# Kernel tuning notes

Hardware: AMD Instinct MI355X
Metric: run time of the kernel (lower is better)

The kernel has to match this reference:

```python
import jax, jax.numpy as jnp
import numpy as np

BEV_H = 150; BEV_W = 150; D = 4; NCAM = 6; C = 128
FH = 48; FW = 88            # camera feature map size
IMG_H = 480.0; IMG_W = 800.0  # raw image size used to normalize uv
PC = np.array([-51.2, -51.2, -5.0, 51.2, 51.2, 3.0], np.float32)  # pc_range


def setup_inputs() -> dict:
    key = jax.random.key(0)
    # GenerateGrid buffer: (D, 3, h, w) with channels (x, y, z), normalized to [0,1]
    z = PC[5] - PC[2]
    zs = (np.linspace(0.5, z - 0.5, D) / z).astype(np.float32)
    xs = (np.linspace(0.5, BEV_W - 0.5, BEV_W) / BEV_W).astype(np.float32)
    ys = (np.linspace(0.5, BEV_H - 0.5, BEV_H) / BEV_H).astype(np.float32)
    g = np.zeros((D, 3, BEV_H, BEV_W), np.float32)
    g[:, 0] = xs[None, None, :]
    g[:, 1] = ys[None, :, None]
    g[:, 2] = zs[:, None, None]
    # realistic surround-camera rig: 6 cams looking outward every 60 deg
    I = np.zeros((1, NCAM, 3, 3), np.float32)
    E = np.zeros((1, NCAM, 4, 4), np.float32)
    for i in range(NCAM):
        I[0, i] = [[500.0, 0.0, 400.0], [0.0, 500.0, 240.0], [0.0, 0.0, 1.0]]
        yaw = 2.0 * np.pi * i / NCAM
        fwd = np.array([np.cos(yaw), np.sin(yaw), 0.0])
        right = np.array([np.sin(yaw), -np.cos(yaw), 0.0])
        down = np.array([0.0, 0.0, -1.0])
        R = np.stack([right, down, fwd])  # rows = camera axes in ego frame
        campos = np.array([1.5 * np.cos(yaw), 1.5 * np.sin(yaw), 1.5])
        E[0, i, :3, :3] = R
        E[0, i, :3, 3] = -R @ campos
        E[0, i, 3, 3] = 1.0
    feat = jax.random.normal(key, (1, NCAM, FH, FW, C), jnp.float32)
    return {"feat": feat, "I": jnp.asarray(I), "E": jnp.asarray(E), "grid_3d": jnp.asarray(g)}


def _forward(feat, I, E, grid_3d):
    b, n = I.shape[:2]
    d, _, h, w = grid_3d.shape
    Q = h * w
    scale = jnp.asarray([PC[3] - PC[0], PC[4] - PC[1], PC[5] - PC[2]], feat.dtype)
    off = jnp.asarray([PC[0], PC[1], PC[2]], feat.dtype)
    # (D, Q, 3) ego-frame 3D reference points, then homogeneous (D, Q, 4)
    rp = grid_3d.reshape(d, 3, Q).transpose(0, 2, 1) * scale + off
    rp4 = jnp.concatenate([rp, jnp.ones((d, Q, 1), rp.dtype)], axis=-1)
    # lidar2img = I @ E[:, :, :3, :] -> (b, n, 3, 4); project -> (b, n, D, Q, 3)
    l2i = jnp.einsum('bnij,bnjk->bnik', I, E[:, :, :3, :])
    proj = jnp.einsum('bnij,dqj->bndqi', l2i, rp4)
    eps = 1e-5
    zc = proj[..., 2]
    mask = zc > eps
    uv = proj[..., :2] / jnp.maximum(zc, eps)[..., None]
    u = uv[..., 0] / IMG_W
    v = uv[..., 1] / IMG_H
    mask = mask & (u > 0.0) & (u < 1.0) & (v > 0.0) & (v < 1.0)
    # bilinear grid_sample (align_corners=False, zero padding) at (u, v)
    px = u * FW - 0.5
    py = v * FH - 0.5
    x0 = jnp.floor(px)
    y0 = jnp.floor(py)
    wx1 = px - x0; wy1 = py - y0
    wx0 = 1.0 - wx1; wy0 = 1.0 - wy1
    x0i = x0.astype(jnp.int32)
    y0i = y0.astype(jnp.int32)
    ff = feat.reshape(b, n, FH * FW, C)

    def gather(xi, yi, wt):
        valid = (xi >= 0) & (xi < FW) & (yi >= 0) & (yi < FH)
        idx = (jnp.clip(yi, 0, FH - 1) * FW + jnp.clip(xi, 0, FW - 1)).reshape(b, n, d * Q)
        g = jnp.take_along_axis(ff, idx[..., None], axis=2).reshape(b, n, d, Q, C)
        return g * (wt * valid.astype(feat.dtype))[..., None]

    sampled = (gather(x0i, y0i, wx0 * wy0) + gather(x0i + 1, y0i, wx1 * wy0)
               + gather(x0i, y0i + 1, wx0 * wy1) + gather(x0i + 1, y0i + 1, wx1 * wy1))
    # mask-weighted fusion over cameras and pillar points (BEVFormer SCA)
    m = mask.astype(feat.dtype)
    out = jnp.einsum('bndq,bndqc->bqc', m, sampled)
    cnt = jnp.clip(m.sum(axis=(1, 2)), 1.0, None)
    return out / cnt[..., None]  # (b, Q, C)


def reference(feat, I, E, grid_3d):
    return _forward(feat, I, E, grid_3d)
```

## Files before the change

kernel.cpp:

```cpp
#include <hip/hip_runtime.h>

#define BEV_H 150
#define BEV_W 150
#define DD    4
#define NCAM  6
#define CC    128
#define FH    48
#define FW    88
#define IMG_Hf 480.0f
#define IMG_Wf 800.0f
#define NPTS  24

__device__ __forceinline__ float rdlanef(float x, int l) {
    return __uint_as_float((unsigned)__builtin_amdgcn_readlane((int)__float_as_uint(x), l));
}

__global__ __launch_bounds__(128) void bev_sample_kernel(
    const float* __restrict__ feat,
    const float* __restrict__ I_,
    const float* __restrict__ E_,
    const float* __restrict__ grid,
    float* __restrict__ out)
{
    const int tid  = threadIdx.x;
    const int lane = tid & 63;
    const int wv   = tid >> 6;
    const int l32  = lane & 31;
    const bool lowhalf = (lane < 32);

    __shared__ float s_l2i[NCAM][12];
    if (tid < NCAM * 12) {
        const int n = tid / 12, r = tid % 12;
        const int i = r >> 2, j = r & 3;
        float acc = 0.f;
        #pragma unroll
        for (int k = 0; k < 3; ++k)
            acc += I_[n * 9 + i * 3 + k] * E_[n * 16 + k * 4 + j];
        s_l2i[n][r] = acc;
    }
    __syncthreads();

    int p;
    {
        const int b = blockIdx.x;
        const int xcd = b & 7, ii = b >> 3;
        p = (xcd == 0) ? ii : (704 + (xcd - 1) * 703 + ii);
    }
    const int ph = p / 75, pw = p - ph * 75;
    const int h  = ph * 2 + wv;
    const int wA = pw * 2;
    const int qA = h * BEV_W + wA;

    int   iT = 0, iB = 0;
    float wTL = 0.f, wTR = 0.f, wBL = 0.f, wBR = 0.f;
    bool  m = false;

    const bool actA = (lane < NPTS);
    const bool actB = (lane >= 32) && (lane < 32 + NPTS);
    if (actA || actB) {
        const int n = l32 >> 2;
        const int d = l32 & 3;
        const int wc = wA + (actB ? 1 : 0);

        const float gx = grid[((d * 3 + 0) * BEV_H + h) * BEV_W + wc];
        const float gy = grid[((d * 3 + 1) * BEV_H + h) * BEV_W + wc];
        const float gz = grid[((d * 3 + 2) * BEV_H + h) * BEV_W + wc];
        const float x = gx * 102.4f - 51.2f;
        const float y = gy * 102.4f - 51.2f;
        const float z = gz * 8.0f   - 5.0f;

        const float4 M0 = *(const float4*)&s_l2i[n][0];
        const float4 M1 = *(const float4*)&s_l2i[n][4];
        const float4 M2 = *(const float4*)&s_l2i[n][8];
        const float p0 = M0.x * x + M0.y * y + M0.z * z + M0.w;
        const float p1 = M1.x * x + M1.y * y + M1.z * z + M1.w;
        const float p2 = M2.x * x + M2.y * y + M2.z * z + M2.w;

        const float eps = 1e-5f;
        const float zc = fmaxf(p2, eps);
        const float u = (p0 / zc) * (1.0f / IMG_Wf);
        const float v = (p1 / zc) * (1.0f / IMG_Hf);
        m = (p2 > eps) && (u > 0.f) && (u < 1.f) && (v > 0.f) && (v < 1.f);

        const float px = u * (float)FW - 0.5f;
        const float py = v * (float)FH - 0.5f;
        const float fx0 = floorf(px), fy0 = floorf(py);
        const int x0 = (int)fx0, y0 = (int)fy0;
        const int x1 = x0 + 1,   y1 = y0 + 1;
        const float wx1 = px - fx0, wy1 = py - fy0;
        const float wx0 = 1.f - wx1, wy0 = 1.f - wy1;

        const bool vx0 = (x0 >= 0) && (x0 < FW);
        const bool vx1 = (x1 >= 0) && (x1 < FW);
        const bool vy0 = (y0 >= 0) && (y0 < FH);
        const bool vy1 = (y1 >= 0) && (y1 < FH);
        const int cx0 = min(max(x0, 0), FW - 1), cx1 = min(max(x1, 0), FW - 1);
        const int cy0 = min(max(y0, 0), FH - 1), cy1 = min(max(y1, 0), FH - 1);

        const float w0v = wx0 * wy0 * ((vx0 && vy0) ? 1.f : 0.f);
        const float w1v = wx1 * wy0 * ((vx1 && vy0) ? 1.f : 0.f);
        const float w2v = wx0 * wy1 * ((vx0 && vy1) ? 1.f : 0.f);
        const float w3v = wx1 * wy1 * ((vx1 && vy1) ? 1.f : 0.f);

        const int bx = min(max(x0, 0), FW - 2);
        wTL = ((cx0 == bx)     ? w0v : 0.f) + ((cx1 == bx)     ? w1v : 0.f);
        wTR = ((cx0 == bx + 1) ? w0v : 0.f) + ((cx1 == bx + 1) ? w1v : 0.f);
        wBL = ((cx0 == bx)     ? w2v : 0.f) + ((cx1 == bx)     ? w3v : 0.f);
        wBR = ((cx0 == bx + 1) ? w2v : 0.f) + ((cx1 == bx + 1) ? w3v : 0.f);

        const int base = n * FH * FW;
        iT = (base + cy0 * FW + bx) * CC;
        iB = (base + cy1 * FW + bx) * CC;
    }

    const unsigned long long bal = __ballot(m);
    unsigned long long balA = bal & 0xFFFFFFull;
    unsigned long long balB = (bal >> 32) & 0xFFFFFFull;
    const float cntA = fmaxf((float)__popcll(balA), 1.f);
    const float cntB = fmaxf((float)__popcll(balB), 1.f);

    float aAx = 0.f, aAy = 0.f, aAz = 0.f, aAw = 0.f;
    float aBx = 0.f, aBy = 0.f, aBz = 0.f, aBw = 0.f;
    const int loff = 4 * lane;

    while (balA | balB) {
        int eA0 = 0, eA1 = 0, eB0 = 32, eB1 = 32;
        float sA0 = 0.f, sA1 = 0.f, sB0 = 0.f, sB1 = 0.f;
        if (balA) {
            eA0 = (int)__builtin_ctzll(balA); balA &= balA - 1; sA0 = 1.f;
            if (balA) { eA1 = (int)__builtin_ctzll(balA); balA &= balA - 1; sA1 = 1.f; }
            else eA1 = eA0;
        }
        if (balB) {
            eB0 = 32 + (int)__builtin_ctzll(balB); balB &= balB - 1; sB0 = 1.f;
            if (balB) { eB1 = 32 + (int)__builtin_ctzll(balB); balB &= balB - 1; sB1 = 1.f; }
            else eB1 = eB0;
        }

        const int jTA0 = __builtin_amdgcn_readlane(iT, eA0), jBA0 = __builtin_amdgcn_readlane(iB, eA0);
        const int jTA1 = __builtin_amdgcn_readlane(iT, eA1), jBA1 = __builtin_amdgcn_readlane(iB, eA1);
        const int jTB0 = __builtin_amdgcn_readlane(iT, eB0), jBB0 = __builtin_amdgcn_readlane(iB, eB0);
        const int jTB1 = __builtin_amdgcn_readlane(iT, eB1), jBB1 = __builtin_amdgcn_readlane(iB, eB1);

        const float4 fTA0 = *(const float4*)(feat + jTA0 + loff);
        const float4 fBA0 = *(const float4*)(feat + jBA0 + loff);
        const float4 fTA1 = *(const float4*)(feat + jTA1 + loff);
        const float4 fBA1 = *(const float4*)(feat + jBA1 + loff);
        const float4 fTB0 = *(const float4*)(feat + jTB0 + loff);
        const float4 fBB0 = *(const float4*)(feat + jBB0 + loff);
        const float4 fTB1 = *(const float4*)(feat + jTB1 + loff);
        const float4 fBB1 = *(const float4*)(feat + jBB1 + loff);

        const float wTA0 = sA0 * (lowhalf ? rdlanef(wTL, eA0) : rdlanef(wTR, eA0));
        const float wBA0 = sA0 * (lowhalf ? rdlanef(wBL, eA0) : rdlanef(wBR, eA0));
        const float wTA1 = sA1 * (lowhalf ? rdlanef(wTL, eA1) : rdlanef(wTR, eA1));
        const float wBA1 = sA1 * (lowhalf ? rdlanef(wBL, eA1) : rdlanef(wBR, eA1));
        const float wTB0 = sB0 * (lowhalf ? rdlanef(wTL, eB0) : rdlanef(wTR, eB0));
        const float wBB0 = sB0 * (lowhalf ? rdlanef(wBL, eB0) : rdlanef(wBR, eB0));
        const float wTB1 = sB1 * (lowhalf ? rdlanef(wTL, eB1) : rdlanef(wTR, eB1));
        const float wBB1 = sB1 * (lowhalf ? rdlanef(wBL, eB1) : rdlanef(wBR, eB1));

        aAx += wTA0 * fTA0.x + wBA0 * fBA0.x + wTA1 * fTA1.x + wBA1 * fBA1.x;
        aAy += wTA0 * fTA0.y + wBA0 * fBA0.y + wTA1 * fTA1.y + wBA1 * fBA1.y;
        aAz += wTA0 * fTA0.z + wBA0 * fBA0.z + wTA1 * fTA1.z + wBA1 * fBA1.z;
        aAw += wTA0 * fTA0.w + wBA0 * fBA0.w + wTA1 * fTA1.w + wBA1 * fBA1.w;
        aBx += wTB0 * fTB0.x + wBB0 * fBB0.x + wTB1 * fTB1.x + wBB1 * fBB1.x;
        aBy += wTB0 * fTB0.y + wBB0 * fBB0.y + wTB1 * fTB1.y + wBB1 * fBB1.y;
        aBz += wTB0 * fTB0.z + wBB0 * fBB0.z + wTB1 * fTB1.z + wBB1 * fBB1.z;
        aBw += wTB0 * fTB0.w + wBB0 * fBB0.w + wTB1 * fTB1.w + wBB1 * fBB1.w;
    }

    aAx += __shfl_xor(aAx, 32);  aAy += __shfl_xor(aAy, 32);
    aAz += __shfl_xor(aAz, 32);  aAw += __shfl_xor(aAw, 32);
    aBx += __shfl_xor(aBx, 32);  aBy += __shfl_xor(aBy, 32);
    aBz += __shfl_xor(aBz, 32);  aBw += __shfl_xor(aBw, 32);

    const float inv = lowhalf ? (1.f / cntA) : (1.f / cntB);
    const int   q   = lowhalf ? qA : (qA + 1);
    float4 o;
    o.x = (lowhalf ? aAx : aBx) * inv;
    o.y = (lowhalf ? aAy : aBy) * inv;
    o.z = (lowhalf ? aAz : aBz) * inv;
    o.w = (lowhalf ? aAw : aBw) * inv;
    *(float4*)(out + q * CC + 4 * l32) = o;
}

extern "C" void kernel_launch(void* const* d_in, const int* in_sizes, int n_in,
                              void* d_out, int out_size, void* d_ws, size_t ws_size,
                              hipStream_t stream) {
    const float* feat = (const float*)d_in[0];
    const float* I_   = (const float*)d_in[1];
    const float* E_   = (const float*)d_in[2];
    const float* grid = (const float*)d_in[3];
    float* out        = (float*)d_out;

    bev_sample_kernel<<<(BEV_H / 2) * (BEV_W / 2), 128, 0, stream>>>(feat, I_, E_, grid, out);
}
```

Before: 19.84 us.

## Software-pipeline feature gathers and remap blocks to 2D tiles per XCD

The gather loop is now software-pipelined: the next iteration's feature loads and weight readlanes are issued before the current batch is accumulated, so memory latency overlaps with FMAs. Separately, the block-to-BEV mapping now gives each XCD a contiguous 2D tile (two row bands by four column strips) instead of a linear range, which is meant to improve L2 locality of the camera features each XCD touches. The grid is padded to 8*722 blocks and surplus blocks exit early. Holding two batches of loads in flight costs extra registers and may lower occupancy.

```diff
diff --git a/kernel.cpp b/kernel.cpp
--- a/kernel.cpp
+++ b/kernel.cpp
@@ -2,7 +2,6 @@
 
 #define BEV_H 150
 #define BEV_W 150
-#define DD    4
 #define NCAM  6
 #define CC    128
 #define FH    48
@@ -13,6 +12,65 @@
 
 __device__ __forceinline__ float rdlanef(float x, int l) {
     return __uint_as_float((unsigned)__builtin_amdgcn_readlane((int)__float_as_uint(x), l));
+}
+
+struct Trip {
+    float4 fTA0, fBA0, fTA1, fBA1, fTB0, fBB0, fTB1, fBB1;
+    float  wTA0, wBA0, wTA1, wBA1, wTB0, wBB0, wTB1, wBB1;
+};
+
+__device__ __forceinline__ void extract2(unsigned& bal, int base,
+                                         int& e0, int& e1, float& s0, float& s1) {
+    e0 = base; e1 = base; s0 = 0.f; s1 = 0.f;
+    if (bal) {
+        e0 = base + __builtin_ctz(bal); bal &= bal - 1; s0 = 1.f;
+        if (bal) { e1 = base + __builtin_ctz(bal); bal &= bal - 1; s1 = 1.f; }
+        else e1 = e0;
+    }
+}
+
+__device__ __forceinline__ Trip issue(int eA0, int eA1, int eB0, int eB1,
+                                      float sA0, float sA1, float sB0, float sB1,
+                                      int iT, int iB,
+                                      float wTL, float wTR, float wBL, float wBR,
+                                      const float* __restrict__ feat, int loff, bool lowhalf) {
+    Trip t;
+    const int jTA0 = __builtin_amdgcn_readlane(iT, eA0), jBA0 = __builtin_amdgcn_readlane(iB, eA0);
+    const int jTA1 = __builtin_amdgcn_readlane(iT, eA1), jBA1 = __builtin_amdgcn_readlane(iB, eA1);
+    const int jTB0 = __builtin_amdgcn_readlane(iT, eB0), jBB0 = __builtin_amdgcn_readlane(iB, eB0);
+    const int jTB1 = __builtin_amdgcn_readlane(iT, eB1), jBB1 = __builtin_amdgcn_readlane(iB, eB1);
+
+    t.fTA0 = *(const float4*)(feat + jTA0 + loff);
+    t.fBA0 = *(const float4*)(feat + jBA0 + loff);
+    t.fTA1 = *(const float4*)(feat + jTA1 + loff);
+    t.fBA1 = *(const float4*)(feat + jBA1 + loff);
+    t.fTB0 = *(const float4*)(feat + jTB0 + loff);
+    t.fBB0 = *(const float4*)(feat + jBB0 + loff);
+    t.fTB1 = *(const float4*)(feat + jTB1 + loff);
+    t.fBB1 = *(const float4*)(feat + jBB1 + loff);
+
+    t.wTA0 = sA0 * (lowhalf ? rdlanef(wTL, eA0) : rdlanef(wTR, eA0));
+    t.wBA0 = sA0 * (lowhalf ? rdlanef(wBL, eA0) : rdlanef(wBR, eA0));
+    t.wTA1 = sA1 * (lowhalf ? rdlanef(wTL, eA1) : rdlanef(wTR, eA1));
+    t.wBA1 = sA1 * (lowhalf ? rdlanef(wBL, eA1) : rdlanef(wBR, eA1));
+    t.wTB0 = sB0 * (lowhalf ? rdlanef(wTL, eB0) : rdlanef(wTR, eB0));
+    t.wBB0 = sB0 * (lowhalf ? rdlanef(wBL, eB0) : rdlanef(wBR, eB0));
+    t.wTB1 = sB1 * (lowhalf ? rdlanef(wTL, eB1) : rdlanef(wTR, eB1));
+    t.wBB1 = sB1 * (lowhalf ? rdlanef(wBL, eB1) : rdlanef(wBR, eB1));
+    return t;
+}
+
+__device__ __forceinline__ void consume(const Trip& t,
+                                        float& aAx, float& aAy, float& aAz, float& aAw,
+                                        float& aBx, float& aBy, float& aBz, float& aBw) {
+    aAx += t.wTA0 * t.fTA0.x + t.wBA0 * t.fBA0.x + t.wTA1 * t.fTA1.x + t.wBA1 * t.fBA1.x;
+    aAy += t.wTA0 * t.fTA0.y + t.wBA0 * t.fBA0.y + t.wTA1 * t.fTA1.y + t.wBA1 * t.fBA1.y;
+    aAz += t.wTA0 * t.fTA0.z + t.wBA0 * t.fBA0.z + t.wTA1 * t.fTA1.z + t.wBA1 * t.fBA1.z;
+    aAw += t.wTA0 * t.fTA0.w + t.wBA0 * t.fBA0.w + t.wTA1 * t.fTA1.w + t.wBA1 * t.fBA1.w;
+    aBx += t.wTB0 * t.fTB0.x + t.wBB0 * t.fBB0.x + t.wTB1 * t.fTB1.x + t.wBB1 * t.fBB1.x;
+    aBy += t.wTB0 * t.fTB0.y + t.wBB0 * t.fBB0.y + t.wTB1 * t.fTB1.y + t.wBB1 * t.fBB1.y;
+    aBz += t.wTB0 * t.fTB0.z + t.wBB0 * t.fBB0.z + t.wTB1 * t.fTB1.z + t.wBB1 * t.fBB1.z;
+    aBw += t.wTB0 * t.fTB0.w + t.wBB0 * t.fBB0.w + t.wTB1 * t.fTB1.w + t.wBB1 * t.fBB1.w;
 }
 
 __global__ __launch_bounds__(128) void bev_sample_kernel(
@@ -28,7 +86,7 @@
     const int l32  = lane & 31;
     const bool lowhalf = (lane < 32);
 
-    __shared__ float s_l2i[NCAM][12];
+    __shared__ __align__(16) float s_l2i[NCAM][12];
     if (tid < NCAM * 12) {
         const int n = tid / 12, r = tid % 12;
         const int i = r >> 2, j = r & 3;
@@ -40,13 +98,19 @@
     }
     __syncthreads();
 
-    int p;
-    {
-        const int b = blockIdx.x;
-        const int xcd = b & 7, ii = b >> 3;
-        p = (xcd == 0) ? ii : (704 + (xcd - 1) * 703 + ii);
-    }
-    const int ph = p / 75, pw = p - ph * 75;
+    const int r   = blockIdx.x & 7;
+    const int i   = blockIdx.x >> 3;
+    const int row0 = (r < 4) ? 0 : 38;
+    const int nrow = (r < 4) ? 38 : 37;
+    const int c3   = r & 3;
+    const int col0 = c3 * 19;
+    const int wr   = (c3 == 3) ? 18 : 19;
+    if (i >= nrow * wr) return;
+    int ph, pw;
+    if (wr == 19) { ph = i / 19; pw = i - ph * 19; }
+    else          { ph = i / 18; pw = i - ph * 18; }
+    ph += row0; pw += col0;
+
     const int h  = ph * 2 + wv;
     const int wA = pw * 2;
     const int qA = h * BEV_W + wA;
@@ -114,61 +178,31 @@
     }
 
     const unsigned long long bal = __ballot(m);
-    unsigned long long balA = bal & 0xFFFFFFull;
-    unsigned long long balB = (bal >> 32) & 0xFFFFFFull;
-    const float cntA = fmaxf((float)__popcll(balA), 1.f);
-    const float cntB = fmaxf((float)__popcll(balB), 1.f);
+    unsigned balA = (unsigned)(bal & 0xFFFFFFull);
+    unsigned balB = (unsigned)((bal >> 32) & 0xFFFFFFull);
+    const float cntA = fmaxf((float)__popc(balA), 1.f);
+    const float cntB = fmaxf((float)__popc(balB), 1.f);
 
     float aAx = 0.f, aAy = 0.f, aAz = 0.f, aAw = 0.f;
     float aBx = 0.f, aBy = 0.f, aBz = 0.f, aBw = 0.f;
     const int loff = 4 * lane;
+    const bool any = (balA | balB) != 0u;
+
+    int eA0, eA1, eB0, eB1; float sA0, sA1, sB0, sB1;
+    extract2(balA, 0,  eA0, eA1, sA0, sA1);
+    extract2(balB, 32, eB0, eB1, sB0, sB1);
+    Trip cur = issue(eA0, eA1, eB0, eB1, sA0, sA1, sB0, sB1,
+                     iT, iB, wTL, wTR, wBL, wBR, feat, loff, lowhalf);
 
     while (balA | balB) {
-        int eA0 = 0, eA1 = 0, eB0 = 32, eB1 = 32;
-        float sA0 = 0.f, sA1 = 0.f, sB0 = 0.f, sB1 = 0.f;
-        if (balA) {
-            eA0 = (int)__builtin_ctzll(balA); balA &= balA - 1; sA0 = 1.f;
-            if (balA) { eA1 = (int)__builtin_ctzll(balA); balA &= balA - 1; sA1 = 1.f; }
-            else eA1 = eA0;
-        }
-        if (balB) {
-            eB0 = 32 + (int)__builtin_ctzll(balB); balB &= balB - 1; sB0 = 1.f;
-            if (balB) { eB1 = 32 + (int)__builtin_ctzll(balB); balB &= balB - 1; sB1 = 1.f; }
-            else eB1 = eB0;
-        }
-
-        const int jTA0 = __builtin_amdgcn_readlane(iT, eA0), jBA0 = __builtin_amdgcn_readlane(iB, eA0);
-        const int jTA1 = __builtin_amdgcn_readlane(iT, eA1), jBA1 = __builtin_amdgcn_readlane(iB, eA1);
-        const int jTB0 = __builtin_amdgcn_readlane(iT, eB0), jBB0 = __builtin_amdgcn_readlane(iB, eB0);
-        const int jTB1 = __builtin_amdgcn_readlane(iT, eB1), jBB1 = __builtin_amdgcn_readlane(iB, eB1);
-
-        const float4 fTA0 = *(const float4*)(feat + jTA0 + loff);
-        const float4 fBA0 = *(const float4*)(feat + jBA0 + loff);
-        const float4 fTA1 = *(const float4*)(feat + jTA1 + loff);
-        const float4 fBA1 = *(const float4*)(feat + jBA1 + loff);
-        const float4 fTB0 = *(const float4*)(feat + jTB0 + loff);
-        const float4 fBB0 = *(const float4*)(feat + jBB0 + loff);
-        const float4 fTB1 = *(const float4*)(feat + jTB1 + loff);
-        const float4 fBB1 = *(const float4*)(feat + jBB1 + loff);
-
-        const float wTA0 = sA0 * (lowhalf ? rdlanef(wTL, eA0) : rdlanef(wTR, eA0));
-        const float wBA0 = sA0 * (lowhalf ? rdlanef(wBL, eA0) : rdlanef(wBR, eA0));
-        const float wTA1 = sA1 * (lowhalf ? rdlanef(wTL, eA1) : rdlanef(wTR, eA1));
-        const float wBA1 = sA1 * (lowhalf ? rdlanef(wBL, eA1) : rdlanef(wBR, eA1));
-        const float wTB0 = sB0 * (lowhalf ? rdlanef(wTL, eB0) : rdlanef(wTR, eB0));
-        const float wBB0 = sB0 * (lowhalf ? rdlanef(wBL, eB0) : rdlanef(wBR, eB0));
-        const float wTB1 = sB1 * (lowhalf ? rdlanef(wTL, eB1) : rdlanef(wTR, eB1));
-        const float wBB1 = sB1 * (lowhalf ? rdlanef(wBL, eB1) : rdlanef(wBR, eB1));
-
-        aAx += wTA0 * fTA0.x + wBA0 * fBA0.x + wTA1 * fTA1.x + wBA1 * fBA1.x;
-        aAy += wTA0 * fTA0.y + wBA0 * fBA0.y + wTA1 * fTA1.y + wBA1 * fBA1.y;
-        aAz += wTA0 * fTA0.z + wBA0 * fBA0.z + wTA1 * fTA1.z + wBA1 * fBA1.z;
-        aAw += wTA0 * fTA0.w + wBA0 * fBA0.w + wTA1 * fTA1.w + wBA1 * fBA1.w;
-        aBx += wTB0 * fTB0.x + wBB0 * fBB0.x + wTB1 * fTB1.x + wBB1 * fBB1.x;
-        aBy += wTB0 * fTB0.y + wBB0 * fBB0.y + wTB1 * fTB1.y + wBB1 * fBB1.y;
-        aBz += wTB0 * fTB0.z + wBB0 * fBB0.z + wTB1 * fTB1.z + wBB1 * fBB1.z;
-        aBw += wTB0 * fTB0.w + wBB0 * fBB0.w + wTB1 * fTB1.w + wBB1 * fBB1.w;
-    }
+        extract2(balA, 0,  eA0, eA1, sA0, sA1);
+        extract2(balB, 32, eB0, eB1, sB0, sB1);
+        Trip nxt = issue(eA0, eA1, eB0, eB1, sA0, sA1, sB0, sB1,
+                         iT, iB, wTL, wTR, wBL, wBR, feat, loff, lowhalf);
+        consume(cur, aAx, aAy, aAz, aAw, aBx, aBy, aBz, aBw);
+        cur = nxt;
+    }
+    if (any) consume(cur, aAx, aAy, aAz, aAw, aBx, aBy, aBz, aBw);
 
     aAx += __shfl_xor(aAx, 32);  aAy += __shfl_xor(aAy, 32);
     aAz += __shfl_xor(aAz, 32);  aAw += __shfl_xor(aAw, 32);
@@ -194,5 +228,5 @@
     const float* grid = (const float*)d_in[3];
     float* out        = (float*)d_out;
 
-    bev_sample_kernel<<<(BEV_H / 2) * (BEV_W / 2), 128, 0, stream>>>(feat, I_, E_, grid, out);
-}
+    bev_sample_kernel<<<8 * 722, 128, 0, stream>>>(feat, I_, E_, grid, out);
+}
```

Measured after the change: 21.00 us. 5.8% more time.

## Convert features to bf16 in a pre-pass and gather bf16 in sampler

Applied to the files above, without the earlier changes.

Adds a separate kernel that rounds the fp32 camera feature map to bf16 in workspace, then the sampling kernel gathers 8-byte bf16 chunks instead of 16-byte fp32 chunks and widens them back to fp32 for accumulation. The aim is to halve gather bandwidth and cache footprint. It also issues the grid loads before the shared-memory matrix setup barrier, narrows the ballot masks to 32-bit, and sets an occupancy hint. The cost is an extra full pass over the feature map each call, which writes the workspace, plus a second launch and reduced precision in the sampled values.

```diff
diff --git a/kernel.cpp b/kernel.cpp
--- a/kernel.cpp
+++ b/kernel.cpp
@@ -2,7 +2,6 @@
 
 #define BEV_H 150
 #define BEV_W 150
-#define DD    4
 #define NCAM  6
 #define CC    128
 #define FH    48
@@ -10,13 +9,34 @@
 #define IMG_Hf 480.0f
 #define IMG_Wf 800.0f
 #define NPTS  24
+#define NPIX  (NCAM * FH * FW)
 
 __device__ __forceinline__ float rdlanef(float x, int l) {
     return __uint_as_float((unsigned)__builtin_amdgcn_readlane((int)__float_as_uint(x), l));
 }
 
-__global__ __launch_bounds__(128) void bev_sample_kernel(
-    const float* __restrict__ feat,
+__global__ __launch_bounds__(256) void conv_bf16_kernel(
+    const float* __restrict__ in, unsigned short* __restrict__ out16)
+{
+    const int i = blockIdx.x * 256 + threadIdx.x;
+    const int n4 = NPIX * CC / 4;
+    if (i < n4) {
+        const float4 v = ((const float4*)in)[i];
+        unsigned a = __float_as_uint(v.x), b = __float_as_uint(v.y);
+        unsigned c = __float_as_uint(v.z), d = __float_as_uint(v.w);
+        a = (a + 0x7fffu + ((a >> 16) & 1u)) >> 16;
+        b = (b + 0x7fffu + ((b >> 16) & 1u)) >> 16;
+        c = (c + 0x7fffu + ((c >> 16) & 1u)) >> 16;
+        d = (d + 0x7fffu + ((d >> 16) & 1u)) >> 16;
+        uint2 o; o.x = a | (b << 16); o.y = c | (d << 16);
+        ((uint2*)out16)[i] = o;
+    }
+}
+
+template <bool BF16>
+__global__ __launch_bounds__(128, 4) void bev_sample_kernel(
+    const float* __restrict__ featf,
+    const unsigned short* __restrict__ feat16,
     const float* __restrict__ I_,
     const float* __restrict__ E_,
     const float* __restrict__ grid,
@@ -28,18 +48,6 @@
     const int l32  = lane & 31;
     const bool lowhalf = (lane < 32);
 
-    __shared__ float s_l2i[NCAM][12];
-    if (tid < NCAM * 12) {
-        const int n = tid / 12, r = tid % 12;
-        const int i = r >> 2, j = r & 3;
-        float acc = 0.f;
-        #pragma unroll
-        for (int k = 0; k < 3; ++k)
-            acc += I_[n * 9 + i * 3 + k] * E_[n * 16 + k * 4 + j];
-        s_l2i[n][r] = acc;
-    }
-    __syncthreads();
-
     int p;
     {
         const int b = blockIdx.x;
@@ -51,20 +59,36 @@
     const int wA = pw * 2;
     const int qA = h * BEV_W + wA;
 
+    const bool actA = (lane < NPTS);
+    const bool actB = (lane >= 32) && (lane < 32 + NPTS);
+    float gx = 0.f, gy = 0.f, gz = 0.f;
+    int n = 0;
+    if (actA || actB) {
+        n = l32 >> 2;
+        const int d = l32 & 3;
+        const int wc = wA + (actB ? 1 : 0);
+        gx = grid[((d * 3 + 0) * BEV_H + h) * BEV_W + wc];
+        gy = grid[((d * 3 + 1) * BEV_H + h) * BEV_W + wc];
+        gz = grid[((d * 3 + 2) * BEV_H + h) * BEV_W + wc];
+    }
+
+    __shared__ __align__(16) float s_l2i[NCAM][12];
+    if (tid < NCAM * 12) {
+        const int nn = tid / 12, r = tid % 12;
+        const int i = r >> 2, j = r & 3;
+        float acc = 0.f;
+        #pragma unroll
+        for (int k = 0; k < 3; ++k)
+            acc += I_[nn * 9 + i * 3 + k] * E_[nn * 16 + k * 4 + j];
+        s_l2i[nn][r] = acc;
+    }
+    __syncthreads();
+
     int   iT = 0, iB = 0;
     float wTL = 0.f, wTR = 0.f, wBL = 0.f, wBR = 0.f;
     bool  m = false;
 
-    const bool actA = (lane < NPTS);
-    const bool actB = (lane >= 32) && (lane < 32 + NPTS);
     if (actA || actB) {
-        const int n = l32 >> 2;
-        const int d = l32 & 3;
-        const int wc = wA + (actB ? 1 : 0);
-
-        const float gx = grid[((d * 3 + 0) * BEV_H + h) * BEV_W + wc];
-        const float gy = grid[((d * 3 + 1) * BEV_H + h) * BEV_W + wc];
-        const float gz = grid[((d * 3 + 2) * BEV_H + h) * BEV_W + wc];
         const float x = gx * 102.4f - 51.2f;
         const float y = gy * 102.4f - 51.2f;
         const float z = gz * 8.0f   - 5.0f;
@@ -114,10 +138,10 @@
     }
 
     const unsigned long long bal = __ballot(m);
-    unsigned long long balA = bal & 0xFFFFFFull;
-    unsigned long long balB = (bal >> 32) & 0xFFFFFFull;
-    const float cntA = fmaxf((float)__popcll(balA), 1.f);
-    const float cntB = fmaxf((float)__popcll(balB), 1.f);
+    unsigned balA = (unsigned)(bal & 0xFFFFFFull);
+    unsigned balB = (unsigned)((bal >> 32) & 0xFFFFFFull);
+    const float cntA = fmaxf((float)__popc(balA), 1.f);
+    const float cntB = fmaxf((float)__popc(balB), 1.f);
 
     float aAx = 0.f, aAy = 0.f, aAz = 0.f, aAw = 0.f;
     float aBx = 0.f, aBy = 0.f, aBz = 0.f, aBw = 0.f;
@@ -127,13 +151,13 @@
         int eA0 = 0, eA1 = 0, eB0 = 32, eB1 = 32;
         float sA0 = 0.f, sA1 = 0.f, sB0 = 0.f, sB1 = 0.f;
         if (balA) {
-            eA0 = (int)__builtin_ctzll(balA); balA &= balA - 1; sA0 = 1.f;
-            if (balA) { eA1 = (int)__builtin_ctzll(balA); balA &= balA - 1; sA1 = 1.f; }
+            eA0 = __builtin_ctz(balA); balA &= balA - 1; sA0 = 1.f;
+            if (balA) { eA1 = __builtin_ctz(balA); balA &= balA - 1; sA1 = 1.f; }
             else eA1 = eA0;
         }
         if (balB) {
-            eB0 = 32 + (int)__builtin_ctzll(balB); balB &= balB - 1; sB0 = 1.f;
-            if (balB) { eB1 = 32 + (int)__builtin_ctzll(balB); balB &= balB - 1; sB1 = 1.f; }
+            eB0 = 32 + __builtin_ctz(balB); balB &= balB - 1; sB0 = 1.f;
+            if (balB) { eB1 = 32 + __builtin_ctz(balB); balB &= balB - 1; sB1 = 1.f; }
             else eB1 = eB0;
         }
 
@@ -141,15 +165,6 @@
         const int jTA1 = __builtin_amdgcn_readlane(iT, eA1), jBA1 = __builtin_amdgcn_readlane(iB, eA1);
         const int jTB0 = __builtin_amdgcn_readlane(iT, eB0), jBB0 = __builtin_amdgcn_readlane(iB, eB0);
         const int jTB1 = __builtin_amdgcn_readlane(iT, eB1), jBB1 = __builtin_amdgcn_readlane(iB, eB1);
-
-        const float4 fTA0 = *(const float4*)(feat + jTA0 + loff);
-        const float4 fBA0 = *(const float4*)(feat + jBA0 + loff);
-        const float4 fTA1 = *(const float4*)(feat + jTA1 + loff);
-        const float4 fBA1 = *(const float4*)(feat + jBA1 + loff);
-        const float4 fTB0 = *(const float4*)(feat + jTB0 + loff);
-        const float4 fBB0 = *(const float4*)(feat + jBB0 + loff);
-        const float4 fTB1 = *(const float4*)(feat + jTB1 + loff);
-        const float4 fBB1 = *(const float4*)(feat + jBB1 + loff);
 
         const float wTA0 = sA0 * (lowhalf ? rdlanef(wTL, eA0) : rdlanef(wTR, eA0));
         const float wBA0 = sA0 * (lowhalf ? rdlanef(wBL, eA0) : rdlanef(wBR, eA0));
@@ -160,14 +175,48 @@
         const float wTB1 = sB1 * (lowhalf ? rdlanef(wTL, eB1) : rdlanef(wTR, eB1));
         const float wBB1 = sB1 * (lowhalf ? rdlanef(wBL, eB1) : rdlanef(wBR, eB1));
 
-        aAx += wTA0 * fTA0.x + wBA0 * fBA0.x + wTA1 * fTA1.x + wBA1 * fBA1.x;
-        aAy += wTA0 * fTA0.y + wBA0 * fBA0.y + wTA1 * fTA1.y + wBA1 * fBA1.y;
-        aAz += wTA0 * fTA0.z + wBA0 * fBA0.z + wTA1 * fTA1.z + wBA1 * fBA1.z;
-        aAw += wTA0 * fTA0.w + wBA0 * fBA0.w + wTA1 * fTA1.w + wBA1 * fBA1.w;
-        aBx += wTB0 * fTB0.x + wBB0 * fBB0.x + wTB1 * fTB1.x + wBB1 * fBB1.x;
-        aBy += wTB0 * fTB0.y + wBB0 * fBB0.y + wTB1 * fTB1.y + wBB1 * fBB1.y;
-        aBz += wTB0 * fTB0.z + wBB0 * fBB0.z + wTB1 * fTB1.z + wBB1 * fBB1.z;
-        aBw += wTB0 * fTB0.w + wBB0 * fBB0.w + wTB1 * fTB1.w + wBB1 * fBB1.w;
+        if constexpr (BF16) {
+            const uint2 dTA0 = *(const uint2*)(feat16 + jTA0 + loff);
+            const uint2 dBA0 = *(const uint2*)(feat16 + jBA0 + loff);
+            const uint2 dTA1 = *(const uint2*)(feat16 + jTA1 + loff);
+            const uint2 dBA1 = *(const uint2*)(feat16 + jBA1 + loff);
+            const uint2 dTB0 = *(const uint2*)(feat16 + jTB0 + loff);
+            const uint2 dBB0 = *(const uint2*)(feat16 + jBB0 + loff);
+            const uint2 dTB1 = *(const uint2*)(feat16 + jTB1 + loff);
+            const uint2 dBB1 = *(const uint2*)(feat16 + jBB1 + loff);
+
+            #define ACC4(dd, ww, a0, a1, a2, a3)                              \
+                a0 += (ww) * __uint_as_float((dd).x << 16);                   \
+                a1 += (ww) * __uint_as_float((dd).x & 0xffff0000u);           \
+                a2 += (ww) * __uint_as_float((dd).y << 16);                   \
+                a3 += (ww) * __uint_as_float((dd).y & 0xffff0000u);
+            ACC4(dTA0, wTA0, aAx, aAy, aAz, aAw)
+            ACC4(dBA0, wBA0, aAx, aAy, aAz, aAw)
+            ACC4(dTA1, wTA1, aAx, aAy, aAz, aAw)
+            ACC4(dBA1, wBA1, aAx, aAy, aAz, aAw)
+            ACC4(dTB0, wTB0, aBx, aBy, aBz, aBw)
+            ACC4(dBB0, wBB0, aBx, aBy, aBz, aBw)
+            ACC4(dTB1, wTB1, aBx, aBy, aBz, aBw)
+            ACC4(dBB1, wBB1, aBx, aBy, aBz, aBw)
+            #undef ACC4
+        } else {
+            const float4 fTA0 = *(const float4*)(featf + jTA0 + loff);
+            const float4 fBA0 = *(const float4*)(featf + jBA0 + loff);
+            const float4 fTA1 = *(const float4*)(featf + jTA1 + loff);
+            const float4 fBA1 = *(const float4*)(featf + jBA1 + loff);
+            const float4 fTB0 = *(const float4*)(featf + jTB0 + loff);
+            const float4 fBB0 = *(const float4*)(featf + jBB0 + loff);
+            const float4 fTB1 = *(const float4*)(featf + jTB1 + loff);
+            const float4 fBB1 = *(const float4*)(featf + jBB1 + loff);
+            aAx += wTA0 * fTA0.x + wBA0 * fBA0.x + wTA1 * fTA1.x + wBA1 * fBA1.x;
+            aAy += wTA0 * fTA0.y + wBA0 * fBA0.y + wTA1 * fTA1.y + wBA1 * fBA1.y;
+            aAz += wTA0 * fTA0.z + wBA0 * fBA0.z + wTA1 * fTA1.z + wBA1 * fBA1.z;
+            aAw += wTA0 * fTA0.w + wBA0 * fBA0.w + wTA1 * fTA1.w + wBA1 * fBA1.w;
+            aBx += wTB0 * fTB0.x + wBB0 * fBB0.x + wTB1 * fTB1.x + wBB1 * fBB1.x;
+            aBy += wTB0 * fTB0.y + wBB0 * fBB0.y + wTB1 * fTB1.y + wBB1 * fBB1.y;
+            aBz += wTB0 * fTB0.z + wBB0 * fBB0.z + wTB1 * fTB1.z + wBB1 * fBB1.z;
+            aBw += wTB0 * fTB0.w + wBB0 * fBB0.w + wTB1 * fTB1.w + wBB1 * fBB1.w;
+        }
     }
 
     aAx += __shfl_xor(aAx, 32);  aAy += __shfl_xor(aAy, 32);
@@ -194,5 +243,15 @@
     const float* grid = (const float*)d_in[3];
     float* out        = (float*)d_out;
 
-    bev_sample_kernel<<<(BEV_H / 2) * (BEV_W / 2), 128, 0, stream>>>(feat, I_, E_, grid, out);
-}
+    const size_t need = (size_t)NPIX * CC * sizeof(unsigned short);
+    if (ws_size >= need) {
+        unsigned short* f16 = (unsigned short*)d_ws;
+        const int n4 = NPIX * CC / 4;
+        conv_bf16_kernel<<<(n4 + 255) / 256, 256, 0, stream>>>(feat, f16);
+        bev_sample_kernel<true><<<(BEV_H / 2) * (BEV_W / 2), 128, 0, stream>>>(
+            feat, f16, I_, E_, grid, out);
+    } else {
+        bev_sample_kernel<false><<<(BEV_H / 2) * (BEV_W / 2), 128, 0, stream>>>(
+            feat, (const unsigned short*)nullptr, I_, E_, grid, out);
+    }
+}
```

Result: slower. 26.79 us (+35.0%).

## Remap blocks to 2D BEV tiles per XCD and hoist grid loads before sync

Applied to the files above, without the earlier changes.

Changes the block-to-BEV mapping so each of the 8 XCDs handles a compact 2D rectangular tile of the BEV grid instead of a contiguous run of rows. Neighbouring BEV points project to nearby camera features, so this aims to improve L2 locality per XCD. The grid loads are moved ahead of the shared-memory l2i setup and barrier so their latency overlaps it, and the ballot masks use 32-bit ops. The grid grows to 8*722 blocks, a few of which exit early.

```diff
diff --git a/kernel.cpp b/kernel.cpp
--- a/kernel.cpp
+++ b/kernel.cpp
@@ -2,7 +2,6 @@
 
 #define BEV_H 150
 #define BEV_W 150
-#define DD    4
 #define NCAM  6
 #define CC    128
 #define FH    48
@@ -28,43 +27,53 @@
     const int l32  = lane & 31;
     const bool lowhalf = (lane < 32);
 
-    __shared__ float s_l2i[NCAM][12];
+    const int r    = blockIdx.x & 7;
+    const int i    = blockIdx.x >> 3;
+    const int row0 = (r < 4) ? 0 : 38;
+    const int nrow = (r < 4) ? 38 : 37;
+    const int c3   = r & 3;
+    const int col0 = c3 * 19;
+    const int wr   = (c3 == 3) ? 18 : 19;
+    if (i >= nrow * wr) return;
+    int ph, pw;
+    if (wr == 19) { ph = i / 19; pw = i - ph * 19; }
+    else          { ph = i / 18; pw = i - ph * 18; }
+    ph += row0; pw += col0;
+
+    const int h  = ph * 2 + wv;
+    const int wA = pw * 2;
+    const int qA = h * BEV_W + wA;
+
+    const bool actA = (lane < NPTS);
+    const bool actB = (lane >= 32) && (lane < 32 + NPTS);
+    float gx = 0.f, gy = 0.f, gz = 0.f;
+    int n = 0;
+    if (actA || actB) {
+        n = l32 >> 2;
+        const int d = l32 & 3;
+        const int wc = wA + (actB ? 1 : 0);
+        gx = grid[((d * 3 + 0) * BEV_H + h) * BEV_W + wc];
+        gy = grid[((d * 3 + 1) * BEV_H + h) * BEV_W + wc];
+        gz = grid[((d * 3 + 2) * BEV_H + h) * BEV_W + wc];
+    }
+
+    __shared__ __align__(16) float s_l2i[NCAM][12];
     if (tid < NCAM * 12) {
-        const int n = tid / 12, r = tid % 12;
-        const int i = r >> 2, j = r & 3;
+        const int nn = tid / 12, rr = tid % 12;
+        const int ii = rr >> 2, j = rr & 3;
         float acc = 0.f;
         #pragma unroll
         for (int k = 0; k < 3; ++k)
-            acc += I_[n * 9 + i * 3 + k] * E_[n * 16 + k * 4 + j];
-        s_l2i[n][r] = acc;
+            acc += I_[nn * 9 + ii * 3 + k] * E_[nn * 16 + k * 4 + j];
+        s_l2i[nn][rr] = acc;
     }
     __syncthreads();
-
-    int p;
-    {
-        const int b = blockIdx.x;
-        const int xcd = b & 7, ii = b >> 3;
-        p = (xcd == 0) ? ii : (704 + (xcd - 1) * 703 + ii);
-    }
-    const int ph = p / 75, pw = p - ph * 75;
-    const int h  = ph * 2 + wv;
-    const int wA = pw * 2;
-    const int qA = h * BEV_W + wA;
 
     int   iT = 0, iB = 0;
     float wTL = 0.f, wTR = 0.f, wBL = 0.f, wBR = 0.f;
     bool  m = false;
 
-    const bool actA = (lane < NPTS);
-    const bool actB = (lane >= 32) && (lane < 32 + NPTS);
     if (actA || actB) {
-        const int n = l32 >> 2;
-        const int d = l32 & 3;
-        const int wc = wA + (actB ? 1 : 0);
-
-        const float gx = grid[((d * 3 + 0) * BEV_H + h) * BEV_W + wc];
-        const float gy = grid[((d * 3 + 1) * BEV_H + h) * BEV_W + wc];
-        const float gz = grid[((d * 3 + 2) * BEV_H + h) * BEV_W + wc];
         const float x = gx * 102.4f - 51.2f;
         const float y = gy * 102.4f - 51.2f;
         const float z = gz * 8.0f   - 5.0f;
@@ -114,10 +123,10 @@
     }
 
     const unsigned long long bal = __ballot(m);
-    unsigned long long balA = bal & 0xFFFFFFull;
-    unsigned long long balB = (bal >> 32) & 0xFFFFFFull;
-    const float cntA = fmaxf((float)__popcll(balA), 1.f);
-    const float cntB = fmaxf((float)__popcll(balB), 1.f);
+    unsigned balA = (unsigned)(bal & 0xFFFFFFull);
+    unsigned balB = (unsigned)((bal >> 32) & 0xFFFFFFull);
+    const float cntA = fmaxf((float)__popc(balA), 1.f);
+    const float cntB = fmaxf((float)__popc(balB), 1.f);
 
     float aAx = 0.f, aAy = 0.f, aAz = 0.f, aAw = 0.f;
     float aBx = 0.f, aBy = 0.f, aBz = 0.f, aBw = 0.f;
@@ -127,13 +136,13 @@
         int eA0 = 0, eA1 = 0, eB0 = 32, eB1 = 32;
         float sA0 = 0.f, sA1 = 0.f, sB0 = 0.f, sB1 = 0.f;
         if (balA) {
-            eA0 = (int)__builtin_ctzll(balA); balA &= balA - 1; sA0 = 1.f;
-            if (balA) { eA1 = (int)__builtin_ctzll(balA); balA &= balA - 1; sA1 = 1.f; }
+            eA0 = __builtin_ctz(balA); balA &= balA - 1; sA0 = 1.f;
+            if (balA) { eA1 = __builtin_ctz(balA); balA &= balA - 1; sA1 = 1.f; }
             else eA1 = eA0;
         }
         if (balB) {
-            eB0 = 32 + (int)__builtin_ctzll(balB); balB &= balB - 1; sB0 = 1.f;
-            if (balB) { eB1 = 32 + (int)__builtin_ctzll(balB); balB &= balB - 1; sB1 = 1.f; }
+            eB0 = 32 + __builtin_ctz(balB); balB &= balB - 1; sB0 = 1.f;
+            if (balB) { eB1 = 32 + __builtin_ctz(balB); balB &= balB - 1; sB1 = 1.f; }
             else eB1 = eB0;
         }
 
@@ -194,5 +203,5 @@
     const float* grid = (const float*)d_in[3];
     float* out        = (float*)d_out;
 
-    bev_sample_kernel<<<(BEV_H / 2) * (BEV_W / 2), 128, 0, stream>>>(feat, I_, E_, grid, out);
+    bev_sample_kernel<<<8 * 722, 128, 0, stream>>>(feat, I_, E_, grid, out);
 }
```

Measured after the change: 18.95 us. 1.05x faster.
